# Optimization experiments

Measured on AMD Instinct MI355X. Metric: run time of the kernel, lower is better.

The kernel has to match this reference:

```python
import jax, jax.numpy as jnp
import numpy as np

D_MODEL = 1024
NUM_HEADS = 16
THETA = 10000.0


def _rope(x, positions):
    # x: [..., S, d_k] with interleaved even/odd pairs; positions: [S] int
    d_k = x.shape[-1]
    inv_freq = 1.0 / (THETA ** (jnp.arange(0, d_k, 2, dtype=jnp.float32) / d_k))  # [d_k/2]
    freqs = positions.astype(jnp.float32)[:, None] * inv_freq[None, :]  # [S, d_k/2]
    cos = jnp.cos(freqs)
    sin = jnp.sin(freqs)
    x_even = x[..., 0::2]
    x_odd = x[..., 1::2]
    rot_even = x_even * cos - x_odd * sin
    rot_odd = x_even * sin + x_odd * cos
    out = jnp.stack([rot_even, rot_odd], axis=-1)  # [..., S, d_k/2, 2]
    return out.reshape(x.shape)


def setup_inputs() -> dict:
    key = jax.random.key(0)
    k1, k2, k3 = jax.random.split(key, 3)
    B, S = 2, 2048
    x = jax.random.normal(k1, (B, S, D_MODEL), dtype=jnp.float32)
    Wqkv = jax.random.normal(k2, (3 * D_MODEL, D_MODEL), dtype=jnp.float32) * (D_MODEL ** -0.5)
    Wout = jax.random.normal(k3, (D_MODEL, D_MODEL), dtype=jnp.float32) * (D_MODEL ** -0.5)
    token_positions = jnp.arange(S, dtype=jnp.int32)
    return {"x": x, "Wqkv": Wqkv, "Wout": Wout, "token_positions": token_positions}


def reference(x, Wqkv, Wout, token_positions):
    B, S, D = x.shape
    H = NUM_HEADS
    d_k = D // H
    qkv = x @ Wqkv.T  # [B, S, 3D]
    qkv = qkv.reshape(B, S, 3, H, d_k).transpose(0, 2, 3, 1, 4)  # [B, 3, H, S, d_k]
    q, k, v = qkv[:, 0], qkv[:, 1], qkv[:, 2]  # each [B, H, S, d_k]
    q = _rope(q, token_positions)
    k = _rope(k, token_positions)
    scores = jnp.einsum("bhqd,bhkd->bhqk", q, k) / jnp.sqrt(jnp.float32(d_k))
    attn = jax.nn.softmax(scores, axis=-1)
    out = jnp.einsum("bhqk,bhkd->bhqd", attn, v)  # [B, H, S, d_k]
    out = out.transpose(0, 2, 1, 3).reshape(B, S, D)
    return out @ Wout.T
```

## Files before the change

kernel.cpp:

```cpp
#include <hip/hip_runtime.h>
#include <stdint.h>

typedef unsigned short u16;
typedef unsigned int u32;
typedef __bf16 bf16x8 __attribute__((ext_vector_type(8)));
typedef float f32x4 __attribute__((ext_vector_type(4)));
typedef float f32x16 __attribute__((ext_vector_type(16)));

#define MFMA16 __builtin_amdgcn_mfma_f32_16x16x32_bf16
#define MFMA32 __builtin_amdgcn_mfma_f32_32x32x16_bf16

static __device__ __forceinline__ u16 f2bf(float f) {
  union { float f; u32 u; } v; v.f = f;
  u32 r = v.u + 0x7FFFu + ((v.u >> 16) & 1u);
  return (u16)(r >> 16);
}
static __device__ __forceinline__ float bf2f(u16 b) {
  union { float f; u32 u; } v; v.u = ((u32)b) << 16;
  return v.f;
}
static __device__ __forceinline__ void load_lds16(const void* g, void* l) {
  __builtin_amdgcn_global_load_lds(
      (const __attribute__((address_space(1))) void*)g,
      (__attribute__((address_space(3))) void*)l, 16, 0, 0);
}

__global__ __launch_bounds__(256) void cvt_bf16(const float* __restrict__ in,
                                                u16* __restrict__ out, int n4) {
  int i = blockIdx.x * 256 + threadIdx.x;
  if (i >= n4) return;
  float4 v = reinterpret_cast<const float4*>(in)[i];
  uint2 r;
  r.x = (u32)f2bf(v.x) | ((u32)f2bf(v.y) << 16);
  r.y = (u32)f2bf(v.z) | ((u32)f2bf(v.w) << 16);
  reinterpret_cast<uint2*>(out)[i] = r;
}

template <bool OUT_BF16>
__global__ __launch_bounds__(256, 2) void gemm_bt(const u16* __restrict__ A,
                                                  const u16* __restrict__ B,
                                                  void* __restrict__ Cv,
                                                  int M, int N, int K) {
  __shared__ u16 As[128 * 32];
  __shared__ u16 Bs[128 * 32];
  const int t = threadIdx.x;
  const int w = t >> 6, lane = t & 63;
  const int brow = blockIdx.y * 128, bcol = blockIdx.x * 128;
  const int wr = (w >> 1) * 64, wc = (w & 1) * 64;

  f32x4 acc[4][4];
#pragma unroll
  for (int i = 0; i < 4; ++i)
#pragma unroll
    for (int j = 0; j < 4; ++j) acc[i][j] = (f32x4){0.f, 0.f, 0.f, 0.f};

  const int srow = w * 16 + (lane >> 2);
  const int scol = (lane & 3) * 8;
  const u16* ga = A + (size_t)(brow + srow) * K + scol;
  const u16* gb = B + (size_t)(bcol + srow) * K + scol;
  const size_t rstep = (size_t)64 * K;
  u16* ldsA = As + w * 512;
  u16* ldsB = Bs + w * 512;

  const int lc = lane & 15, lg = lane >> 4;
  const int kg = lg * 8;

  const int nk = K >> 5;
  for (int kt = 0; kt < nk; ++kt) {
    __syncthreads();
    load_lds16(ga, ldsA);
    load_lds16(ga + rstep, (char*)ldsA + 4096);
    load_lds16(gb, ldsB);
    load_lds16(gb + rstep, (char*)ldsB + 4096);
    ga += 32; gb += 32;
    asm volatile("s_waitcnt vmcnt(0)" ::: "memory");
    __syncthreads();
    bf16x8 af[4], bfr[4];
#pragma unroll
    for (int i = 0; i < 4; ++i)
      af[i] = *reinterpret_cast<const bf16x8*>(As + (wr + i * 16 + lc) * 32 + kg);
#pragma unroll
    for (int j = 0; j < 4; ++j)
      bfr[j] = *reinterpret_cast<const bf16x8*>(Bs + (wc + j * 16 + lc) * 32 + kg);
#pragma unroll
    for (int i = 0; i < 4; ++i)
#pragma unroll
      for (int j = 0; j < 4; ++j)
        acc[i][j] = MFMA16(af[i], bfr[j], acc[i][j], 0, 0, 0);
  }

  const int r0 = lg * 4;
#pragma unroll
  for (int i = 0; i < 4; ++i)
#pragma unroll
    for (int j = 0; j < 4; ++j)
#pragma unroll
      for (int r = 0; r < 4; ++r) {
        const int m = brow + wr + i * 16 + r0 + r;
        const int n = bcol + wc + j * 16 + lc;
        if constexpr (OUT_BF16)
          ((u16*)Cv)[(size_t)m * N + n] = f2bf(acc[i][j][r]);
        else
          ((float*)Cv)[(size_t)m * N + n] = acc[i][j][r];
      }
}

__global__ __launch_bounds__(256) void build_trig(const int* __restrict__ pos,
                                                  float2* __restrict__ tab) {
  int i = blockIdx.x * 256 + threadIdx.x;
  int s = i >> 5, p = i & 31;
  float inv = powf(10000.0f, -(float)p * (1.0f / 32.0f));
  float fr = (float)pos[s] * inv;
  float sn, cs;
  sincosf(fr, &sn, &cs);
  tab[i] = make_float2(cs, sn);
}

__global__ __launch_bounds__(256) void rope_repack(const u16* __restrict__ qkv,
                                                   const float2* __restrict__ tab,
                                                   u16* __restrict__ Qro,
                                                   u16* __restrict__ Kro) {
  int idx = blockIdx.x * 256 + threadIdx.x;
  int p = idx & 31;
  int h = (idx >> 5) & 15;
  int m = idx >> 9;
  int b = m >> 11, s = m & 2047;
  const u32* row = reinterpret_cast<const u32*>(qkv + (size_t)m * 3072);
  u32 qp = row[h * 32 + p];
  u32 kp = row[512 + h * 32 + p];
  float2 cssn = tab[s * 32 + p];
  float cs = cssn.x, sn = cssn.y;
  float qe = bf2f((u16)(qp & 0xffffu)), qo = bf2f((u16)(qp >> 16));
  float ke = bf2f((u16)(kp & 0xffffu)), ko = bf2f((u16)(kp >> 16));
  const float QS = 0.18033688011112042f;
  float qre = (qe * cs - qo * sn) * QS;
  float qro_ = (qe * sn + qo * cs) * QS;
  float kre = ke * cs - ko * sn;
  float kro_ = ke * sn + ko * cs;
  size_t o = ((size_t)(b * 16 + h) * 2048 + s) * 32 + p;
  reinterpret_cast<u32*>(Qro)[o] = (u32)f2bf(qre) | ((u32)f2bf(qro_) << 16);
  reinterpret_cast<u32*>(Kro)[o] = (u32)f2bf(kre) | ((u32)f2bf(kro_) << 16);
}

__global__ __launch_bounds__(256) void v_transpose(const u16* __restrict__ qkv,
                                                   u16* __restrict__ VT) {
  const int bh = blockIdx.y;
  const int s0 = blockIdx.x * 64;
  const int b = bh >> 4, h = bh & 15;
  __shared__ u16 tile[64][72];
  const int t = threadIdx.x;
#pragma unroll
  for (int c = 0; c < 2; ++c) {
    int r = c * 32 + (t >> 3);
    int d = (t & 7) * 8;
    const u16* src = qkv + (size_t)(b * 2048 + s0 + r) * 3072 + 2048 + h * 64 + d;
    *reinterpret_cast<uint4*>(&tile[r][d]) = *reinterpret_cast<const uint4*>(src);
  }
  __syncthreads();
#pragma unroll
  for (int c = 0; c < 2; ++c) {
    int dd = c * 32 + (t >> 3);
    int sg = (t & 7) * 8;
    u16 tmp[8];
#pragma unroll
    for (int jj = 0; jj < 8; ++jj) tmp[jj] = tile[sg + jj][dd];
    *reinterpret_cast<uint4*>(VT + ((size_t)bh * 64 + dd) * 2048 + s0 + sg) =
        *reinterpret_cast<const uint4*>(tmp);
  }
}

__global__ __launch_bounds__(256) void attn_fwd2(const u16* __restrict__ Q,
                                                 const u16* __restrict__ Kg,
                                                 const u16* __restrict__ VTg,
                                                 u16* __restrict__ O) {
  constexpr int S = 2048, NT = 32;
  __shared__ char lds[3][16384];
  const int t = threadIdx.x, wv = t >> 6, lane = t & 63;
  const int bid = blockIdx.x;
  const int slot = bid >> 3;
  const int bh = (bid & 7) * 4 + (slot >> 4);
  const int qb = slot & 15;
  const int b = bh >> 4, h = bh & 15;
  const int q0 = qb * 128 + wv * 32;
  const size_t kbase = (size_t)bh * (S * 64);
  const int l31 = lane & 31, hi = lane >> 5;

  bf16x8 qf[4];
  {
    const u16* qp = Q + kbase + (size_t)(q0 + l31) * 64 + hi * 8;
#pragma unroll
    for (int d = 0; d < 4; ++d)
      qf[d] = *reinterpret_cast<const bf16x8*>(qp + d * 16);
  }

  f32x16 Oacc[2];
#pragma unroll
  for (int i = 0; i < 2; ++i)
#pragma unroll
    for (int r = 0; r < 16; ++r) Oacc[i][r] = 0.f;
  float m = -__builtin_inff(), lsum = 0.f;

  const char* gk0 = (const char*)(Kg + kbase);
  const char* gv0 = (const char*)(VTg + kbase);

#define STAGE(KT, BUF)                                                         \
  {                                                                            \
    char* lk_ = lds[BUF];                                                      \
    const char* gk_ = gk0 + (size_t)(KT) * 8192;                               \
    _Pragma("unroll") for (int c_ = 0; c_ < 2; ++c_) {                         \
      int o_ = (c_ * 256 + t) * 16;                                            \
      int row_ = o_ >> 7, colb_ = o_ & 127;                                    \
      int swz_ = colb_ ^ ((row_ & 7) << 4);                                    \
      load_lds16(gk_ + row_ * 128 + swz_, lk_ + o_);                           \
      load_lds16(gv0 + (size_t)row_ * 4096 + (KT) * 128 + swz_,                \
                 lk_ + 8192 + o_);                                             \
    }                                                                          \
  }

  STAGE(0, 0)
  STAGE(1, 1)
  asm volatile("s_waitcnt vmcnt(4)" ::: "memory");
  __builtin_amdgcn_s_barrier();

  int cur = 0;
  for (int kt = 0; kt < NT; ++kt) {
    const int nxt = kt + 2 < NT ? kt + 2 : NT - 1;
    const int nbuf = cur + 2 >= 3 ? cur - 1 : cur + 2;
    STAGE(nxt, nbuf)
    const char* lk = lds[cur];
    const char* lv = lds[cur] + 8192;

    f32x16 Sa[2];
#pragma unroll
    for (int i = 0; i < 2; ++i)
#pragma unroll
      for (int r = 0; r < 16; ++r) Sa[i][r] = 0.f;
    __builtin_amdgcn_s_setprio(1);
#pragma unroll
    for (int d = 0; d < 4; ++d) {
#pragma unroll
      for (int kvt = 0; kvt < 2; ++kvt) {
        int kv = kvt * 32 + l31;
        int a = (kv * 128 + d * 32 + hi * 16) ^ ((kv & 7) << 4);
        bf16x8 kf = *reinterpret_cast<const bf16x8*>(lk + a);
        Sa[kvt] = MFMA32(kf, qf[d], Sa[kvt], 0, 0, 0);
      }
    }
    __builtin_amdgcn_s_setprio(0);

    float mt[16];
#pragma unroll
    for (int r = 0; r < 16; ++r) mt[r] = fmaxf(Sa[0][r], Sa[1][r]);
#pragma unroll
    for (int d = 8; d >= 1; d >>= 1)
#pragma unroll
      for (int r = 0; r < d; ++r) mt[r] = fmaxf(mt[r], mt[r + d]);
    float pmax = fmaxf(mt[0], __shfl_xor(mt[0], 32));

    if (__any(pmax > m + 6.0f)) {
      float mn = fmaxf(m, pmax);
      float sc = exp2f(m - mn);
      m = mn;
      lsum *= sc;
#pragma unroll
      for (int i = 0; i < 2; ++i)
#pragma unroll
        for (int r = 0; r < 16; ++r) Oacc[i][r] *= sc;
    }

#pragma unroll
    for (int kvt = 0; kvt < 2; ++kvt)
#pragma unroll
      for (int r = 0; r < 16; ++r) Sa[kvt][r] = exp2f(Sa[kvt][r] - m);

    {
      float st[16];
#pragma unroll
      for (int r = 0; r < 16; ++r) st[r] = Sa[0][r] + Sa[1][r];
#pragma unroll
      for (int d = 8; d >= 1; d >>= 1)
#pragma unroll
        for (int r = 0; r < d; ++r) st[r] += st[r + d];
      lsum += st[0];
    }

    bf16x8 pfrag[4];
#pragma unroll
    for (int kvt = 0; kvt < 2; ++kvt)
#pragma unroll
      for (int s1 = 0; s1 < 2; ++s1) {
        u32 X0, X1, Y0, Y1;
        const int c0 = s1 * 8, c1 = c0 + 4;
        asm("v_cvt_pk_bf16_f32 %0, %1, %2"
            : "=v"(X0) : "v"(Sa[kvt][c0 + 0]), "v"(Sa[kvt][c0 + 1]));
        asm("v_cvt_pk_bf16_f32 %0, %1, %2"
            : "=v"(X1) : "v"(Sa[kvt][c0 + 2]), "v"(Sa[kvt][c0 + 3]));
        asm("v_cvt_pk_bf16_f32 %0, %1, %2"
            : "=v"(Y0) : "v"(Sa[kvt][c1 + 0]), "v"(Sa[kvt][c1 + 1]));
        asm("v_cvt_pk_bf16_f32 %0, %1, %2"
            : "=v"(Y1) : "v"(Sa[kvt][c1 + 2]), "v"(Sa[kvt][c1 + 3]));
        asm("v_permlane32_swap_b32 %0, %1" : "+v"(X0), "+v"(Y0));
        asm("v_permlane32_swap_b32 %0, %1" : "+v"(X1), "+v"(Y1));
        union { u32 w[4]; bf16x8 v; } u;
        u.w[0] = X0; u.w[1] = X1; u.w[2] = Y0; u.w[3] = Y1;
        pfrag[kvt * 2 + s1] = u.v;
      }

    __builtin_amdgcn_s_setprio(1);
#pragma unroll
    for (int s = 0; s < 4; ++s) {
#pragma unroll
      for (int dt = 0; dt < 2; ++dt) {
        int d = dt * 32 + l31;
        int a = (d * 128 + s * 32 + hi * 16) ^ ((d & 7) << 4);
        bf16x8 vf = *reinterpret_cast<const bf16x8*>(lv + a);
        Oacc[dt] = MFMA32(vf, pfrag[s], Oacc[dt], 0, 0, 0);
      }
    }
    __builtin_amdgcn_s_setprio(0);

    asm volatile("s_waitcnt vmcnt(4)" ::: "memory");
    __builtin_amdgcn_s_barrier();
    cur = cur + 1 == 3 ? 0 : cur + 1;
  }
#undef STAGE

  const float lfull = lsum + __shfl_xor(lsum, 32);
  const float rdiv = 1.0f / lfull;
  const int srow = q0 + l31;
  u16* orow = O + (size_t)(b * S + srow) * 1024 + h * 64;
#pragma unroll
  for (int dt = 0; dt < 2; ++dt)
#pragma unroll
    for (int c = 0; c < 4; ++c) {
      float v0 = Oacc[dt][4 * c + 0] * rdiv;
      float v1 = Oacc[dt][4 * c + 1] * rdiv;
      float v2 = Oacc[dt][4 * c + 2] * rdiv;
      float v3 = Oacc[dt][4 * c + 3] * rdiv;
      uint2 pk;
      pk.x = (u32)f2bf(v0) | ((u32)f2bf(v1) << 16);
      pk.y = (u32)f2bf(v2) | ((u32)f2bf(v3) << 16);
      *reinterpret_cast<uint2*>(orow + dt * 32 + c * 8 + hi * 4) = pk;
    }
}

extern "C" void kernel_launch(void* const* d_in, const int* in_sizes, int n_in,
                              void* d_out, int out_size, void* d_ws, size_t ws_size,
                              hipStream_t stream) {
  (void)in_sizes; (void)n_in; (void)out_size; (void)ws_size;
  const float* x = (const float*)d_in[0];
  const float* wqkv = (const float*)d_in[1];
  const float* wout = (const float*)d_in[2];
  const int* pos = (const int*)d_in[3];
  float* out = (float*)d_out;

  char* ws = (char*)d_ws;
  u16* xb     = (u16*)(ws);
  u16* wqkvb  = (u16*)(ws + 8388608);
  u16* woutb  = (u16*)(ws + 14680064);
  u16* qkvb   = (u16*)(ws + 16777216);
  u16* qro    = (u16*)(ws + 41943040);
  u16* kro    = (u16*)(ws + 50331648);
  u16* vt     = (u16*)(ws + 58720256);
  u16* attno  = (u16*)(ws + 67108864);
  float2* tab = (float2*)(ws + 75497472);

  cvt_bf16<<<4096, 256, 0, stream>>>(x, xb, 1048576);
  cvt_bf16<<<3072, 256, 0, stream>>>(wqkv, wqkvb, 786432);
  cvt_bf16<<<1024, 256, 0, stream>>>(wout, woutb, 262144);
  build_trig<<<256, 256, 0, stream>>>(pos, tab);
  gemm_bt<true><<<dim3(24, 32), 256, 0, stream>>>(xb, wqkvb, qkvb, 4096, 3072, 1024);
  rope_repack<<<8192, 256, 0, stream>>>(qkvb, tab, qro, kro);
  v_transpose<<<dim3(32, 32), 256, 0, stream>>>(qkvb, vt);
  attn_fwd2<<<512, 256, 0, stream>>>(qro, kro, vt, attno);
  gemm_bt<false><<<dim3(8, 32), 256, 0, stream>>>(attno, woutb, out, 4096, 1024, 1024);
}
```

Baseline: 242.3 us.

## Software-pipeline QK^T of next tile with softmax+PV of current tile

Restructures the attention inner loop so the QK^T MFMAs for tile T+1 are issued before the softmax and PV work for tile T, using two ping-pong score register sets. LDS staging goes from triple to quad buffering with a prefetch distance of three tiles, so K/V for the next QK tile is already resident. The aim is to overlap MFMA work with the exp/max/convert VALU work within a wave. In exchange it holds an extra 32 fp32 accumulators per lane, which may raise register pressure and lower occupancy, and it uses 64KB of LDS per block.

```diff
diff --git a/kernel.cpp b/kernel.cpp
--- a/kernel.cpp
+++ b/kernel.cpp
@@ -169,12 +169,109 @@
   }
 }
 
+
+static __device__ __forceinline__ void qk_tile(const char* lk,
+                                               const bf16x8 (&qf)[4],
+                                               f32x16 (&S)[2], int l31, int hi) {
+#pragma unroll
+  for (int i = 0; i < 2; ++i)
+#pragma unroll
+    for (int r = 0; r < 16; ++r) S[i][r] = 0.f;
+  __builtin_amdgcn_s_setprio(1);
+#pragma unroll
+  for (int d = 0; d < 4; ++d) {
+#pragma unroll
+    for (int kvt = 0; kvt < 2; ++kvt) {
+      int kv = kvt * 32 + l31;
+      int a = (kv * 128 + d * 32 + hi * 16) ^ ((kv & 7) << 4);
+      bf16x8 kf = *reinterpret_cast<const bf16x8*>(lk + a);
+      S[kvt] = MFMA32(kf, qf[d], S[kvt], 0, 0, 0);
+    }
+  }
+  __builtin_amdgcn_s_setprio(0);
+}
+
+static __device__ __forceinline__ void sm_pv(const char* lv, f32x16 (&SA)[2],
+                                             f32x16 (&Oacc)[2], float& m,
+                                             float& lsum, int l31, int hi) {
+  float mt[16];
+#pragma unroll
+  for (int r = 0; r < 16; ++r) mt[r] = fmaxf(SA[0][r], SA[1][r]);
+#pragma unroll
+  for (int d = 8; d >= 1; d >>= 1)
+#pragma unroll
+    for (int r = 0; r < d; ++r) mt[r] = fmaxf(mt[r], mt[r + d]);
+  float pmax = fmaxf(mt[0], __shfl_xor(mt[0], 32));
+
+  if (__any(pmax > m + 6.0f)) {
+    float mn = fmaxf(m, pmax);
+    float sc = exp2f(m - mn);
+    m = mn;
+    lsum *= sc;
+#pragma unroll
+    for (int i = 0; i < 2; ++i)
+#pragma unroll
+      for (int r = 0; r < 16; ++r) Oacc[i][r] *= sc;
+  }
+
+#pragma unroll
+  for (int kvt = 0; kvt < 2; ++kvt)
+#pragma unroll
+    for (int r = 0; r < 16; ++r) SA[kvt][r] = exp2f(SA[kvt][r] - m);
+
+  {
+    float st[16];
+#pragma unroll
+    for (int r = 0; r < 16; ++r) st[r] = SA[0][r] + SA[1][r];
+#pragma unroll
+    for (int d = 8; d >= 1; d >>= 1)
+#pragma unroll
+      for (int r = 0; r < d; ++r) st[r] += st[r + d];
+    lsum += st[0];
+  }
+
+  bf16x8 pfrag[4];
+#pragma unroll
+  for (int kvt = 0; kvt < 2; ++kvt)
+#pragma unroll
+    for (int s1 = 0; s1 < 2; ++s1) {
+      u32 X0, X1, Y0, Y1;
+      const int c0 = s1 * 8, c1 = c0 + 4;
+      asm("v_cvt_pk_bf16_f32 %0, %1, %2"
+          : "=v"(X0) : "v"(SA[kvt][c0 + 0]), "v"(SA[kvt][c0 + 1]));
+      asm("v_cvt_pk_bf16_f32 %0, %1, %2"
+          : "=v"(X1) : "v"(SA[kvt][c0 + 2]), "v"(SA[kvt][c0 + 3]));
+      asm("v_cvt_pk_bf16_f32 %0, %1, %2"
+          : "=v"(Y0) : "v"(SA[kvt][c1 + 0]), "v"(SA[kvt][c1 + 1]));
+      asm("v_cvt_pk_bf16_f32 %0, %1, %2"
+          : "=v"(Y1) : "v"(SA[kvt][c1 + 2]), "v"(SA[kvt][c1 + 3]));
+      asm("v_permlane32_swap_b32 %0, %1" : "+v"(X0), "+v"(Y0));
+      asm("v_permlane32_swap_b32 %0, %1" : "+v"(X1), "+v"(Y1));
+      union { u32 w[4]; bf16x8 v; } u;
+      u.w[0] = X0; u.w[1] = X1; u.w[2] = Y0; u.w[3] = Y1;
+      pfrag[kvt * 2 + s1] = u.v;
+    }
+
+  __builtin_amdgcn_s_setprio(1);
+#pragma unroll
+  for (int s = 0; s < 4; ++s) {
+#pragma unroll
+    for (int dt = 0; dt < 2; ++dt) {
+      int d = dt * 32 + l31;
+      int a = (d * 128 + s * 32 + hi * 16) ^ ((d & 7) << 4);
+      bf16x8 vf = *reinterpret_cast<const bf16x8*>(lv + a);
+      Oacc[dt] = MFMA32(vf, pfrag[s], Oacc[dt], 0, 0, 0);
+    }
+  }
+  __builtin_amdgcn_s_setprio(0);
+}
+
 __global__ __launch_bounds__(256) void attn_fwd2(const u16* __restrict__ Q,
                                                  const u16* __restrict__ Kg,
                                                  const u16* __restrict__ VTg,
                                                  u16* __restrict__ O) {
   constexpr int S = 2048, NT = 32;
-  __shared__ char lds[3][16384];
+  __shared__ char lds[4][16384];
   const int t = threadIdx.x, wv = t >> 6, lane = t & 63;
   const int bid = blockIdx.x;
   const int slot = bid >> 3;
@@ -217,112 +314,33 @@
     }                                                                          \
   }
 
+#define HALF(T, SA, SB, DO_QK)                                                 \
+  {                                                                            \
+    asm volatile("s_waitcnt vmcnt(4)" ::: "memory");                           \
+    __builtin_amdgcn_s_barrier();                                              \
+    int st_ = (T) + 3 < NT ? (T) + 3 : NT - 1;                                 \
+    STAGE(st_, ((T) + 3) & 3)                                                  \
+    if (DO_QK) qk_tile(lds[((T) + 1) & 3], qf, SB, l31, hi);                   \
+    sm_pv(lds[(T) & 3] + 8192, SA, Oacc, m, lsum, l31, hi);                    \
+  }
+
+  f32x16 SaA[2], SaB[2];
+
   STAGE(0, 0)
   STAGE(1, 1)
-  asm volatile("s_waitcnt vmcnt(4)" ::: "memory");
+  STAGE(2, 2)
+  asm volatile("s_waitcnt vmcnt(8)" ::: "memory");
   __builtin_amdgcn_s_barrier();
-
-  int cur = 0;
-  for (int kt = 0; kt < NT; ++kt) {
-    const int nxt = kt + 2 < NT ? kt + 2 : NT - 1;
-    const int nbuf = cur + 2 >= 3 ? cur - 1 : cur + 2;
-    STAGE(nxt, nbuf)
-    const char* lk = lds[cur];
-    const char* lv = lds[cur] + 8192;
-
-    f32x16 Sa[2];
-#pragma unroll
-    for (int i = 0; i < 2; ++i)
-#pragma unroll
-      for (int r = 0; r < 16; ++r) Sa[i][r] = 0.f;
-    __builtin_amdgcn_s_setprio(1);
-#pragma unroll
-    for (int d = 0; d < 4; ++d) {
-#pragma unroll
-      for (int kvt = 0; kvt < 2; ++kvt) {
-        int kv = kvt * 32 + l31;
-        int a = (kv * 128 + d * 32 + hi * 16) ^ ((kv & 7) << 4);
-        bf16x8 kf = *reinterpret_cast<const bf16x8*>(lk + a);
-        Sa[kvt] = MFMA32(kf, qf[d], Sa[kvt], 0, 0, 0);
-      }
-    }
-    __builtin_amdgcn_s_setprio(0);
-
-    float mt[16];
-#pragma unroll
-    for (int r = 0; r < 16; ++r) mt[r] = fmaxf(Sa[0][r], Sa[1][r]);
-#pragma unroll
-    for (int d = 8; d >= 1; d >>= 1)
-#pragma unroll
-      for (int r = 0; r < d; ++r) mt[r] = fmaxf(mt[r], mt[r + d]);
-    float pmax = fmaxf(mt[0], __shfl_xor(mt[0], 32));
-
-    if (__any(pmax > m + 6.0f)) {
-      float mn = fmaxf(m, pmax);
-      float sc = exp2f(m - mn);
-      m = mn;
-      lsum *= sc;
-#pragma unroll
-      for (int i = 0; i < 2; ++i)
-#pragma unroll
-        for (int r = 0; r < 16; ++r) Oacc[i][r] *= sc;
-    }
-
-#pragma unroll
-    for (int kvt = 0; kvt < 2; ++kvt)
-#pragma unroll
-      for (int r = 0; r < 16; ++r) Sa[kvt][r] = exp2f(Sa[kvt][r] - m);
-
-    {
-      float st[16];
-#pragma unroll
-      for (int r = 0; r < 16; ++r) st[r] = Sa[0][r] + Sa[1][r];
-#pragma unroll
-      for (int d = 8; d >= 1; d >>= 1)
-#pragma unroll
-        for (int r = 0; r < d; ++r) st[r] += st[r + d];
-      lsum += st[0];
-    }
-
-    bf16x8 pfrag[4];
-#pragma unroll
-    for (int kvt = 0; kvt < 2; ++kvt)
-#pragma unroll
-      for (int s1 = 0; s1 < 2; ++s1) {
-        u32 X0, X1, Y0, Y1;
-        const int c0 = s1 * 8, c1 = c0 + 4;
-        asm("v_cvt_pk_bf16_f32 %0, %1, %2"
-            : "=v"(X0) : "v"(Sa[kvt][c0 + 0]), "v"(Sa[kvt][c0 + 1]));
-        asm("v_cvt_pk_bf16_f32 %0, %1, %2"
-            : "=v"(X1) : "v"(Sa[kvt][c0 + 2]), "v"(Sa[kvt][c0 + 3]));
-        asm("v_cvt_pk_bf16_f32 %0, %1, %2"
-            : "=v"(Y0) : "v"(Sa[kvt][c1 + 0]), "v"(Sa[kvt][c1 + 1]));
-        asm("v_cvt_pk_bf16_f32 %0, %1, %2"
-            : "=v"(Y1) : "v"(Sa[kvt][c1 + 2]), "v"(Sa[kvt][c1 + 3]));
-        asm("v_permlane32_swap_b32 %0, %1" : "+v"(X0), "+v"(Y0));
-        asm("v_permlane32_swap_b32 %0, %1" : "+v"(X1), "+v"(Y1));
-        union { u32 w[4]; bf16x8 v; } u;
-        u.w[0] = X0; u.w[1] = X1; u.w[2] = Y0; u.w[3] = Y1;
-        pfrag[kvt * 2 + s1] = u.v;
-      }
-
-    __builtin_amdgcn_s_setprio(1);
-#pragma unroll
-    for (int s = 0; s < 4; ++s) {
-#pragma unroll
-      for (int dt = 0; dt < 2; ++dt) {
-        int d = dt * 32 + l31;
-        int a = (d * 128 + s * 32 + hi * 16) ^ ((d & 7) << 4);
-        bf16x8 vf = *reinterpret_cast<const bf16x8*>(lv + a);
-        Oacc[dt] = MFMA32(vf, pfrag[s], Oacc[dt], 0, 0, 0);
-      }
-    }
-    __builtin_amdgcn_s_setprio(0);
-
-    asm volatile("s_waitcnt vmcnt(4)" ::: "memory");
-    __builtin_amdgcn_s_barrier();
-    cur = cur + 1 == 3 ? 0 : cur + 1;
-  }
+  qk_tile(lds[0], qf, SaA, l31, hi);
+
+  for (int u = 0; u < 15; ++u) {
+    const int t0 = 2 * u;
+    HALF(t0, SaA, SaB, true)
+    HALF(t0 + 1, SaB, SaA, true)
+  }
+  HALF(30, SaA, SaB, true)
+  HALF(31, SaB, SaA, false)
+#undef HALF
 #undef STAGE
 
   const float lfull = lsum + __shfl_xor(lsum, 32);
```

New measurement: 230.7 us. -4.8%, faster.
